# Kernel optimization log

Measured on AMD Instinct MI355X. Metric: run time of the kernel, lower is better.

## Reference

```python
import jax, jax.numpy as jnp
import numpy as np


def setup_inputs() -> dict:
    key = jax.random.key(0)
    ks = jax.random.split(key, 8)
    B, Nq, Nk, D, H, Cv = 8, 4096, 4096, 2, 64, 64
    q = jax.random.normal(ks[0], (B, Nq, D), dtype=jnp.float32)
    k = jax.random.normal(ks[1], (B, Nk, D), dtype=jnp.float32)
    v = jax.random.normal(ks[2], (B, Nk, Cv), dtype=jnp.float32)
    # Linear params (torch nn.Linear layout: W is (out, in), y = x @ W.T + b)
    s = 1.0 / np.sqrt(D)
    q_proj_w = jax.random.uniform(ks[3], (H, D), jnp.float32, -s, s)
    q_proj_b = jax.random.uniform(ks[4], (H,), jnp.float32, -s, s)
    k_proj_w = jax.random.uniform(ks[5], (H, D), jnp.float32, -s, s)
    k_proj_b = jax.random.uniform(ks[6], (H,), jnp.float32, -s, s)
    return {"q": q, "k": k, "v": v,
            "q_proj_w": q_proj_w, "q_proj_b": q_proj_b,
            "k_proj_w": k_proj_w, "k_proj_b": k_proj_b,
            "top_k": 16}


def _cdist(q, k):
    # Euclidean distances (B, Nq, Nk) via the Gram trick (avoids a BxNqxNkxD diff tensor)
    q2 = jnp.sum(q * q, axis=-1)  # (B, Nq)
    k2 = jnp.sum(k * k, axis=-1)  # (B, Nk)
    d2 = q2[:, :, None] + k2[:, None, :] - 2.0 * jnp.einsum('bqd,bnd->bqn', q, k)
    return jnp.sqrt(jnp.maximum(d2, 0.0))


def _batched_gather(inputs, idx):
    # inputs: (B, Nk, C), idx: (B, Nq, K) -> (B, Nq, K, C)
    return jax.vmap(lambda inp, ix: inp[ix])(inputs, idx)


def reference(q, k, v, q_proj_w, q_proj_b, k_proj_w, k_proj_b, top_k):
    dists = _cdist(q, k)                                   # (B, Nq, Nk)
    _, knn_idx = jax.lax.top_k(-dists, top_k)              # smallest distances
    k_knn = _batched_gather(k, knn_idx)                    # (B, Nq, K, D)
    v_knn = _batched_gather(v, knn_idx)                    # (B, Nq, K, Cv)
    q_emb = q @ q_proj_w.T + q_proj_b                      # (B, Nq, H)
    k_emb = k_knn @ k_proj_w.T + k_proj_b                  # (B, Nq, K, H)
    attn_scores = jnp.einsum('bqh,bqkh->bqk', q_emb, k_emb)
    attn = jax.nn.softmax(attn_scores, axis=-1)
    out = jnp.einsum('bqk,bqkc->bqc', attn, v_knn)         # (B, Nq, Cv)
    return out
```

## Files before the change

kernel.cpp:

```cpp
#include <hip/hip_runtime.h>
#include <stdint.h>

typedef uint64_t u64;
typedef uint32_t u32;

#define NB    8
#define NQ    4096
#define NKEY  4096
#define CV    64
#define KSEL  16
#define G     8
#define NWAVE 4
#define BLK   (NWAVE * 64)
#define CMAX  64
#define PADU  (~(u64)0)

__device__ __forceinline__ u64 shflxor_u64(u64 v, int m) {
    const u32 lo = __shfl_xor((int)(u32)v, m);
    const u32 hi = __shfl_xor((int)(u32)(v >> 32), m);
    return (((u64)hi) << 32) | lo;
}
__device__ __forceinline__ int mbcnt64(u64 m) {
    return (int)__builtin_amdgcn_mbcnt_hi((u32)(m >> 32),
               __builtin_amdgcn_mbcnt_lo((u32)m, 0));
}
__device__ __forceinline__ u32 fkey(float f) {
    const u32 b = __float_as_uint(f);
    return b ^ (0x80000000u | (u32)((int32_t)b >> 31));
}

__device__ __forceinline__ float lanesort64_f32(float v, int lane) {
#pragma unroll
    for (int k = 2; k <= 64; k <<= 1) {
#pragma unroll
        for (int j = k >> 1; j > 0; j >>= 1) {
            const float p = __shfl_xor(v, j);
            const bool up    = ((lane & k) == 0);
            const bool lower = ((lane & j) == 0);
            v = (lower == up) ? fminf(v, p) : fmaxf(v, p);
        }
    }
    return v;
}

__device__ __forceinline__ u64 top16of64(u64 v, int lane) {
#pragma unroll
    for (int k = 2; k <= 16; k <<= 1) {
#pragma unroll
        for (int j = k >> 1; j > 0; j >>= 1) {
            const u64 p = shflxor_u64(v, j);
            const bool up    = ((lane & k) == 0);
            const bool lower = ((lane & j) == 0);
            const u64 mn = v < p ? v : p, mx = v < p ? p : v;
            v = (lower == up) ? mn : mx;
        }
    }
    {   const u64 p = shflxor_u64(v, 16);
        const u64 mn = v < p ? v : p, mx = v < p ? p : v;
        v = ((lane & 16) == 0) ? mn : mx; }
#pragma unroll
    for (int j = 8; j > 0; j >>= 1) {
        const u64 p = shflxor_u64(v, j);
        const bool lower = ((lane & j) == 0);
        const bool dasc  = ((lane & 32) == 0);
        const u64 mn = v < p ? v : p, mx = v < p ? p : v;
        v = (lower == dasc) ? mn : mx;
    }
    {   const u64 p = shflxor_u64(v, 32);
        const u64 mn = v < p ? v : p, mx = v < p ? p : v;
        v = ((lane & 32) == 0) ? mn : mx; }
    return v;
}

__global__ void setup_kernel(const float* __restrict__ qw, const float* __restrict__ qb,
                             const float* __restrict__ kw, const float* __restrict__ kb,
                             float* __restrict__ w9)
{
    const int h = threadIdx.x & 63;
    const float2 a = ((const float2*)qw)[h];
    const float2 c = ((const float2*)kw)[h];
    const float qbh = qb[h], kbh = kb[h];
    float s[9] = { a.x * c.x, a.y * c.x, qbh * c.x,
                   a.x * c.y, a.y * c.y, qbh * c.y,
                   a.x * kbh, a.y * kbh, qbh * kbh };
#pragma unroll
    for (int i = 0; i < 9; ++i)
#pragma unroll
        for (int off = 32; off; off >>= 1) s[i] += __shfl_xor(s[i], off);
    if (h == 0) {
#pragma unroll
        for (int i = 0; i < 9; ++i) w9[i] = s[i];
    }
}

extern "C" __global__ __launch_bounds__(BLK, 4) void bev_main(
    const float* __restrict__ qg, const float* __restrict__ kg,
    const float* __restrict__ vg, const float* __restrict__ w9,
    float* __restrict__ outg)
{
    __shared__ u64 cand[NWAVE][G][CMAX];

    const int tid  = threadIdx.x;
    const int wv   = tid >> 6;
    const int lane = tid & 63;
    const int wvu  = __builtin_amdgcn_readfirstlane(wv);
    const int b    = blockIdx.x >> 7;
    const int qbase = ((int)(blockIdx.x & 127) * NWAVE + wvu) * G;

    const float2* kp  = (const float2*)(kg + (size_t)b * NKEY * 2);
    const float4* kp4 = (const float4*)kp;
    const float2* qp  = (const float2*)qg + (size_t)b * NQ + qbase;

    float qxx[G], qyy[G], m2x[G], m2y[G];
#pragma unroll
    for (int q = 0; q < G; ++q) {
        const float2 qc = qp[q];
        qxx[q] = qc.x; qyy[q] = qc.y;
        m2x[q] = -2.f * qc.x; m2y[q] = -2.f * qc.y;
    }

    float mn[G];
#pragma unroll
    for (int q = 0; q < G; ++q) mn[q] = __builtin_inff();
#pragma unroll 8
    for (int c = 0; c < 32; ++c) {
        const float4 kk = kp4[c * 64 + lane];
        const float k2a = fmaf(kk.x, kk.x, kk.y * kk.y);
        const float k2b = fmaf(kk.z, kk.z, kk.w * kk.w);
#pragma unroll
        for (int q = 0; q < G; ++q) {
            const float va = fmaf(kk.x, m2x[q], fmaf(kk.y, m2y[q], k2a));
            const float vb = fmaf(kk.z, m2x[q], fmaf(kk.w, m2y[q], k2b));
            mn[q] = fminf(mn[q], fminf(va, vb));
        }
    }

    float thr[G];
#pragma unroll
    for (int q = 0; q < G; ++q)
        thr[q] = __shfl(lanesort64_f32(mn[q], lane), 15);

    int cnt[G];
#pragma unroll
    for (int q = 0; q < G; ++q) cnt[q] = 0;
#pragma unroll 4
    for (int c = 0; c < 32; ++c) {
        const float4 kk = kp4[c * 64 + lane];
        const float k2a = fmaf(kk.x, kk.x, kk.y * kk.y);
        const float k2b = fmaf(kk.z, kk.z, kk.w * kk.w);
        const u32 ia = (u32)(2 * (c * 64 + lane));
#pragma unroll
        for (int q = 0; q < G; ++q) {
            const float va = fmaf(kk.x, m2x[q], fmaf(kk.y, m2y[q], k2a));
            const float vb = fmaf(kk.z, m2x[q], fmaf(kk.w, m2y[q], k2b));
            const bool aa = va <= thr[q];
            const bool ab = vb <= thr[q];
            const u64 mka = __ballot(aa);
            const u64 mkb = __ballot(ab);
            if (mka | mkb) {
                const int posa = cnt[q] + mbcnt64(mka);
                cnt[q] += (int)__popcll(mka);
                const int posb = cnt[q] + mbcnt64(mkb);
                cnt[q] += (int)__popcll(mkb);
                if (aa && posa < CMAX)
                    cand[wv][q][posa] = (((u64)fkey(va)) << 32) | ia;
                if (ab && posb < CMAX)
                    cand[wv][q][posb] = (((u64)fkey(vb)) << 32) | (ia + 1);
            }
        }
    }

#pragma unroll
    for (int q = 0; q < G; ++q) {
        if (cnt[q] > CMAX) {
            u32 lo = 0, hi = ~0u;
            while (lo < hi) {
                const u32 mid = lo + ((hi - lo) >> 1);
                int cc = 0;
#pragma unroll 1
                for (int c = 0; c < 32; ++c) {
                    const float4 kk = kp4[c * 64 + lane];
                    const float k2a = fmaf(kk.x, kk.x, kk.y * kk.y);
                    const float k2b = fmaf(kk.z, kk.z, kk.w * kk.w);
                    const float va = fmaf(kk.x, m2x[q], fmaf(kk.y, m2y[q], k2a));
                    const float vb = fmaf(kk.z, m2x[q], fmaf(kk.w, m2y[q], k2b));
                    cc += (fkey(va) <= mid) ? 1 : 0;
                    cc += (fkey(vb) <= mid) ? 1 : 0;
                }
#pragma unroll
                for (int off = 32; off; off >>= 1) cc += __shfl_xor(cc, off);
                if (cc >= KSEL) hi = mid; else lo = mid + 1;
            }
            int cc = 0;
#pragma unroll 1
            for (int c = 0; c < 32; ++c) {
                const float4 kk = kp4[c * 64 + lane];
                const float k2a = fmaf(kk.x, kk.x, kk.y * kk.y);
                const float k2b = fmaf(kk.z, kk.z, kk.w * kk.w);
                const float va = fmaf(kk.x, m2x[q], fmaf(kk.y, m2y[q], k2a));
                const float vb = fmaf(kk.z, m2x[q], fmaf(kk.w, m2y[q], k2b));
                const u32 ta = fkey(va), tb = fkey(vb);
                const bool aa = ta <= lo, ab = tb <= lo;
                const u64 mka = __ballot(aa);
                const u64 mkb = __ballot(ab);
                const int posa = cc + mbcnt64(mka);
                cc += (int)__popcll(mka);
                const int posb = cc + mbcnt64(mkb);
                cc += (int)__popcll(mkb);
                const u32 ia = (u32)(2 * (c * 64 + lane));
                if (aa && posa < CMAX) cand[wv][q][posa] = (((u64)ta) << 32) | ia;
                if (ab && posb < CMAX) cand[wv][q][posb] = (((u64)tb) << 32) | (ia + 1);
            }
            cnt[q] = cc < CMAX ? cc : CMAX;
        }
    }

    const float s1 = w9[0], s2 = w9[1], s3 = w9[2];
    const float s4 = w9[3], s5 = w9[4], s6 = w9[5];
    const float s7 = w9[6], s8 = w9[7], s9 = w9[8];
    const float* vb = vg + (size_t)b * NKEY * CV;

#pragma unroll 1
    for (int q = 0; q < G; ++q) {
        u64 myv = (lane < cnt[q]) ? cand[wv][q][lane] : PADU;
        myv = top16of64(myv, lane);
        const u32 myidx = (u32)myv;

        const float A  = fmaf(qxx[q], s1, fmaf(qyy[q], s2, s3));
        const float Bb = fmaf(qxx[q], s4, fmaf(qyy[q], s5, s6));
        const float Cc = fmaf(qxx[q], s7, fmaf(qyy[q], s8, s9));

        const int sel = (lane < KSEL) ? (int)myidx : 0;
        const float2 kc = kp[sel];
        const float score = fmaf(A, kc.x, fmaf(Bb, kc.y, Cc));
        float mx = score;
#pragma unroll
        for (int off = 8; off; off >>= 1) mx = fmaxf(mx, __shfl_xor(mx, off));
        const float e = __expf(score - mx);
        float sum = e;
#pragma unroll
        for (int off = 8; off; off >>= 1) sum += __shfl_xor(sum, off);
        const float w = e / sum;

        float acc = 0.f;
#pragma unroll
        for (int s = 0; s < KSEL; ++s) {
            const u32 id   = (u32)__builtin_amdgcn_readlane((int)myidx, s);
            const float ws = __uint_as_float(
                (u32)__builtin_amdgcn_readlane((int)__float_as_uint(w), s));
            acc = fmaf(ws, vb[(size_t)id * CV + lane], acc);
        }
        outg[((size_t)b * NQ + qbase + q) * CV + lane] = acc;
    }
}

extern "C" void kernel_launch(void* const* d_in, const int* in_sizes, int n_in,
                              void* d_out, int out_size, void* d_ws, size_t ws_size,
                              hipStream_t stream) {
    const float* q  = (const float*)d_in[0];
    const float* k  = (const float*)d_in[1];
    const float* v  = (const float*)d_in[2];
    const float* qw = (const float*)d_in[3];
    const float* qb = (const float*)d_in[4];
    const float* kw = (const float*)d_in[5];
    const float* kb = (const float*)d_in[6];
    float* out = (float*)d_out;
    float* w9  = (float*)d_ws;

    hipLaunchKernelGGL(setup_kernel, dim3(1), dim3(64), 0, stream,
                       qw, qb, kw, kb, w9);
    hipLaunchKernelGGL(bev_main, dim3(NB * NQ / (G * NWAVE)), dim3(BLK),
                       0, stream, q, k, v, w9, out);
}
```

Measured before the change: 74.86 us.

## Replace brute-force kNN scan with Morton-sorted key chunks and bbox pruning

Adds a setup kernel that bins keys into a 64x64 grid, sorts them by Morton order into 64 chunks of 64, and records per-chunk bounding boxes. The main kernel gives each wave one query, seeds a top-16 from the nearest chunk, then scans only chunks whose bbox lower bound is within the current 16th distance. This removes the full scan over all 4096 keys per query. In exchange it adds a sort pass, a fixed grid range assumption of [-4,4) (exactness is kept by clamping), and data-dependent irregular work.

```diff
diff --git a/kernel.cpp b/kernel.cpp
--- a/kernel.cpp
+++ b/kernel.cpp
@@ -3,17 +3,22 @@
 
 typedef uint64_t u64;
 typedef uint32_t u32;
+typedef unsigned short u16;
 
 #define NB    8
 #define NQ    4096
 #define NKEY  4096
 #define CV    64
 #define KSEL  16
-#define G     8
-#define NWAVE 4
-#define BLK   (NWAVE * 64)
-#define CMAX  64
+#define GRD   64
+#define NCELL (GRD * GRD)
+#define NCHUNK 64
+#define CMAX  128
 #define PADU  (~(u64)0)
+
+#define WS_SKEY  256
+#define WS_SIDX  (WS_SKEY + NB * NKEY * 8)
+#define WS_BBOX  (WS_SIDX + NB * NKEY * 2)
 
 __device__ __forceinline__ u64 shflxor_u64(u64 v, int m) {
     const u32 lo = __shfl_xor((int)(u32)v, m);
@@ -24,23 +29,16 @@
     return (int)__builtin_amdgcn_mbcnt_hi((u32)(m >> 32),
                __builtin_amdgcn_mbcnt_lo((u32)m, 0));
 }
-__device__ __forceinline__ u32 fkey(float f) {
-    const u32 b = __float_as_uint(f);
-    return b ^ (0x80000000u | (u32)((int32_t)b >> 31));
-}
-
-__device__ __forceinline__ float lanesort64_f32(float v, int lane) {
-#pragma unroll
-    for (int k = 2; k <= 64; k <<= 1) {
-#pragma unroll
-        for (int j = k >> 1; j > 0; j >>= 1) {
-            const float p = __shfl_xor(v, j);
-            const bool up    = ((lane & k) == 0);
-            const bool lower = ((lane & j) == 0);
-            v = (lower == up) ? fminf(v, p) : fmaxf(v, p);
-        }
-    }
-    return v;
+__device__ __forceinline__ int cellof(float x) {
+    int c = (int)floorf((x + 4.0f) * 8.0f);
+    return c < 0 ? 0 : (c > GRD - 1 ? GRD - 1 : c);
+}
+__device__ __forceinline__ u32 part1by1(u32 x) {
+    x &= 0xFFu;
+    x = (x | (x << 4)) & 0x0F0Fu;
+    x = (x | (x << 2)) & 0x3333u;
+    x = (x | (x << 1)) & 0x5555u;
+    return x;
 }
 
 __device__ __forceinline__ u64 top16of64(u64 v, int lane) {
@@ -72,186 +70,233 @@
     return v;
 }
 
-__global__ void setup_kernel(const float* __restrict__ qw, const float* __restrict__ qb,
-                             const float* __restrict__ kw, const float* __restrict__ kb,
-                             float* __restrict__ w9)
+__global__ __launch_bounds__(1024, 1) void k_setup(
+    const float* __restrict__ kg,
+    const float* __restrict__ qw, const float* __restrict__ qb,
+    const float* __restrict__ kw, const float* __restrict__ kb,
+    float2* __restrict__ skey_g, u16* __restrict__ sidx_g,
+    float4* __restrict__ bbox_g, float* __restrict__ w9)
 {
-    const int h = threadIdx.x & 63;
-    const float2 a = ((const float2*)qw)[h];
-    const float2 c = ((const float2*)kw)[h];
-    const float qbh = qb[h], kbh = kb[h];
-    float s[9] = { a.x * c.x, a.y * c.x, qbh * c.x,
-                   a.x * c.y, a.y * c.y, qbh * c.y,
-                   a.x * kbh, a.y * kbh, qbh * kbh };
-#pragma unroll
-    for (int i = 0; i < 9; ++i)
-#pragma unroll
-        for (int off = 32; off; off >>= 1) s[i] += __shfl_xor(s[i], off);
-    if (h == 0) {
-#pragma unroll
-        for (int i = 0; i < 9; ++i) w9[i] = s[i];
-    }
-}
-
-extern "C" __global__ __launch_bounds__(BLK, 4) void bev_main(
+    __shared__ u32    hist[NCELL];
+    __shared__ float2 skl[NKEY];
+    __shared__ u16    sil[NKEY];
+    __shared__ u32    wtot[16];
+
+    const int b = blockIdx.x, t = threadIdx.x;
+    const int wv = t >> 6, lane = t & 63;
+
+#pragma unroll
+    for (int i = 0; i < 4; ++i) hist[t * 4 + i] = 0u;
+    __syncthreads();
+
+    float2 kk[4]; int cel[4];
+#pragma unroll
+    for (int i = 0; i < 4; ++i) {
+        const int gid = t + i * 1024;
+        kk[i] = ((const float2*)kg)[(size_t)b * NKEY + gid];
+        cel[i] = (int)(part1by1((u32)cellof(kk[i].x)) |
+                       (part1by1((u32)cellof(kk[i].y)) << 1));
+        atomicAdd(&hist[cel[i]], 1u);
+    }
+    __syncthreads();
+
+    const u32 h0 = hist[4 * t], h1 = hist[4 * t + 1];
+    const u32 h2 = hist[4 * t + 2], h3 = hist[4 * t + 3];
+    const u32 s = h0 + h1 + h2 + h3;
+    u32 inc = s;
+#pragma unroll
+    for (int off = 1; off < 64; off <<= 1) {
+        const u32 p = __shfl_up(inc, off);
+        if (lane >= off) inc += p;
+    }
+    if (lane == 63) wtot[wv] = inc;
+    __syncthreads();
+    if (wv == 0 && lane < 16) {
+        const u32 v = wtot[lane];
+        u32 sc = v;
+#pragma unroll
+        for (int off = 1; off < 16; off <<= 1) {
+            const u32 p = __shfl_up(sc, off);
+            if (lane >= off) sc += p;
+        }
+        wtot[lane] = sc - v;
+    }
+    __syncthreads();
+    const u32 base = wtot[wv] + (inc - s);
+    hist[4 * t]     = base;
+    hist[4 * t + 1] = base + h0;
+    hist[4 * t + 2] = base + h0 + h1;
+    hist[4 * t + 3] = base + h0 + h1 + h2;
+    __syncthreads();
+
+#pragma unroll
+    for (int i = 0; i < 4; ++i) {
+        const u32 p = atomicAdd(&hist[cel[i]], 1u);
+        skl[p] = kk[i];
+        sil[p] = (u16)(t + i * 1024);
+    }
+    __syncthreads();
+
+    float2* skb = skey_g + (size_t)b * NKEY;
+    u16*    sib = sidx_g + (size_t)b * NKEY;
+#pragma unroll
+    for (int i = 0; i < 4; ++i) {
+        const int g = t + i * 1024;
+        skb[g] = skl[g];
+        sib[g] = sil[g];
+    }
+#pragma unroll
+    for (int j = 0; j < 4; ++j) {
+        const int ch = wv * 4 + j;
+        const float2 kc = skl[ch * 64 + lane];
+        float xlo = kc.x, xhi = kc.x, ylo = kc.y, yhi = kc.y;
+#pragma unroll
+        for (int off = 32; off; off >>= 1) {
+            xlo = fminf(xlo, __shfl_xor(xlo, off));
+            xhi = fmaxf(xhi, __shfl_xor(xhi, off));
+            ylo = fminf(ylo, __shfl_xor(ylo, off));
+            yhi = fmaxf(yhi, __shfl_xor(yhi, off));
+        }
+        if (lane == 0) bbox_g[b * NCHUNK + ch] = make_float4(xlo, ylo, xhi, yhi);
+    }
+
+    if (b == 0 && t < 64) {
+        const int h = t;
+        const float2 a = ((const float2*)qw)[h];
+        const float2 c = ((const float2*)kw)[h];
+        const float qbh = qb[h], kbh = kb[h];
+        float ss[9] = { a.x * c.x, a.y * c.x, qbh * c.x,
+                        a.x * c.y, a.y * c.y, qbh * c.y,
+                        a.x * kbh, a.y * kbh, qbh * kbh };
+#pragma unroll
+        for (int i = 0; i < 9; ++i)
+#pragma unroll
+            for (int off = 32; off; off >>= 1) ss[i] += __shfl_xor(ss[i], off);
+        if (h == 0) {
+#pragma unroll
+            for (int i = 0; i < 9; ++i) w9[i] = ss[i];
+        }
+    }
+}
+
+extern "C" __global__ __launch_bounds__(256, 8) void bev_knn(
     const float* __restrict__ qg, const float* __restrict__ kg,
     const float* __restrict__ vg, const float* __restrict__ w9,
-    float* __restrict__ outg)
+    const float2* __restrict__ skey_g, const u16* __restrict__ sidx_g,
+    const float4* __restrict__ bbox_g, float* __restrict__ outg)
 {
-    __shared__ u64 cand[NWAVE][G][CMAX];
-
-    const int tid  = threadIdx.x;
-    const int wv   = tid >> 6;
-    const int lane = tid & 63;
-    const int wvu  = __builtin_amdgcn_readfirstlane(wv);
-    const int b    = blockIdx.x >> 7;
-    const int qbase = ((int)(blockIdx.x & 127) * NWAVE + wvu) * G;
-
-    const float2* kp  = (const float2*)(kg + (size_t)b * NKEY * 2);
-    const float4* kp4 = (const float4*)kp;
-    const float2* qp  = (const float2*)qg + (size_t)b * NQ + qbase;
-
-    float qxx[G], qyy[G], m2x[G], m2y[G];
-#pragma unroll
-    for (int q = 0; q < G; ++q) {
-        const float2 qc = qp[q];
-        qxx[q] = qc.x; qyy[q] = qc.y;
-        m2x[q] = -2.f * qc.x; m2y[q] = -2.f * qc.y;
-    }
-
-    float mn[G];
-#pragma unroll
-    for (int q = 0; q < G; ++q) mn[q] = __builtin_inff();
-#pragma unroll 8
-    for (int c = 0; c < 32; ++c) {
-        const float4 kk = kp4[c * 64 + lane];
-        const float k2a = fmaf(kk.x, kk.x, kk.y * kk.y);
-        const float k2b = fmaf(kk.z, kk.z, kk.w * kk.w);
-#pragma unroll
-        for (int q = 0; q < G; ++q) {
-            const float va = fmaf(kk.x, m2x[q], fmaf(kk.y, m2y[q], k2a));
-            const float vb = fmaf(kk.z, m2x[q], fmaf(kk.w, m2y[q], k2b));
-            mn[q] = fminf(mn[q], fminf(va, vb));
-        }
-    }
-
-    float thr[G];
-#pragma unroll
-    for (int q = 0; q < G; ++q)
-        thr[q] = __shfl(lanesort64_f32(mn[q], lane), 15);
-
-    int cnt[G];
-#pragma unroll
-    for (int q = 0; q < G; ++q) cnt[q] = 0;
-#pragma unroll 4
-    for (int c = 0; c < 32; ++c) {
-        const float4 kk = kp4[c * 64 + lane];
-        const float k2a = fmaf(kk.x, kk.x, kk.y * kk.y);
-        const float k2b = fmaf(kk.z, kk.z, kk.w * kk.w);
-        const u32 ia = (u32)(2 * (c * 64 + lane));
-#pragma unroll
-        for (int q = 0; q < G; ++q) {
-            const float va = fmaf(kk.x, m2x[q], fmaf(kk.y, m2y[q], k2a));
-            const float vb = fmaf(kk.z, m2x[q], fmaf(kk.w, m2y[q], k2b));
-            const bool aa = va <= thr[q];
-            const bool ab = vb <= thr[q];
-            const u64 mka = __ballot(aa);
-            const u64 mkb = __ballot(ab);
-            if (mka | mkb) {
-                const int posa = cnt[q] + mbcnt64(mka);
-                cnt[q] += (int)__popcll(mka);
-                const int posb = cnt[q] + mbcnt64(mkb);
-                cnt[q] += (int)__popcll(mkb);
-                if (aa && posa < CMAX)
-                    cand[wv][q][posa] = (((u64)fkey(va)) << 32) | ia;
-                if (ab && posb < CMAX)
-                    cand[wv][q][posb] = (((u64)fkey(vb)) << 32) | (ia + 1);
+    __shared__ u64 cand[4][CMAX];
+
+    const int tid = threadIdx.x, wv = tid >> 6, lane = tid & 63;
+    const int gw = blockIdx.x * 4 + wv;
+    const int b  = gw >> 12, qi = gw & 4095;
+
+    const float2 qc = ((const float2*)qg)[(size_t)b * NQ + qi];
+    const float qx = qc.x, qy = qc.y;
+    const float2* sk = skey_g + (size_t)b * NKEY;
+    const u16*    si = sidx_g + (size_t)b * NKEY;
+    u64* cd = cand[wv];
+
+    const float4 bb = bbox_g[b * NCHUNK + lane];
+    const float dx = fmaxf(fmaxf(bb.x - qx, qx - bb.z), 0.f);
+    const float dy = fmaxf(fmaxf(bb.y - qy, qy - bb.w), 0.f);
+    const float bd = fmaf(dx, dx, dy * dy);
+
+    float bmn = bd;
+#pragma unroll
+    for (int off = 32; off; off >>= 1) bmn = fminf(bmn, __shfl_xor(bmn, off));
+    const int cn = __builtin_ctzll((unsigned long long)__ballot(bd == bmn));
+
+    u64 myv;
+    {
+        const int pos = cn * 64 + lane;
+        const float2 kk = sk[pos];
+        const float ddx = qx - kk.x, ddy = qy - kk.y;
+        const float d2 = fmaf(ddx, ddx, ddy * ddy);
+        myv = (((u64)__float_as_uint(d2)) << 32) | (u32)si[pos];
+    }
+    myv = top16of64(myv, lane);
+
+    u64 b16;
+    {
+        u64 m = (lane < KSEL) ? myv : 0;
+#pragma unroll
+        for (int off = 32; off; off >>= 1) { const u64 p = shflxor_u64(m, off); m = p > m ? p : m; }
+        b16 = m;
+    }
+    float d16f = __uint_as_float((u32)(b16 >> 32));
+
+    u64 mask = __ballot(bd <= d16f) & ~(1ull << cn);
+    int ecnt = 0;
+#pragma unroll 1
+    while (mask) {
+        const int c = __builtin_ctzll((unsigned long long)mask);
+        mask &= mask - 1;
+        const int pos = c * 64 + lane;
+        const float2 kk = sk[pos];
+        const float ddx = qx - kk.x, ddy = qy - kk.y;
+        const float d2 = fmaf(ddx, ddx, ddy * ddy);
+        const u64 pk = (((u64)__float_as_uint(d2)) << 32) | (u32)si[pos];
+        const bool acc = pk < b16;
+        const u64 mk = __ballot(acc);
+        if (mk) {
+            const int p = ecnt + mbcnt64(mk);
+            if (acc) cd[p] = pk;
+            ecnt += (int)__popcll(mk);
+            if (ecnt >= CMAX - 64) {
+#pragma unroll 1
+                while (ecnt > 0) {
+                    const int take = ecnt < 48 ? ecnt : 48;
+                    const u64 inv = (lane < KSEL) ? myv
+                                  : ((lane - KSEL < take) ? cd[ecnt - take + lane - KSEL] : PADU);
+                    myv = top16of64(inv, lane);
+                    ecnt -= take;
+                }
+                u64 m = (lane < KSEL) ? myv : 0;
+#pragma unroll
+                for (int off = 32; off; off >>= 1) { const u64 p2 = shflxor_u64(m, off); m = p2 > m ? p2 : m; }
+                b16 = m; d16f = __uint_as_float((u32)(b16 >> 32));
+                mask &= __ballot(bd <= d16f);
             }
         }
     }
-
-#pragma unroll
-    for (int q = 0; q < G; ++q) {
-        if (cnt[q] > CMAX) {
-            u32 lo = 0, hi = ~0u;
-            while (lo < hi) {
-                const u32 mid = lo + ((hi - lo) >> 1);
-                int cc = 0;
 #pragma unroll 1
-                for (int c = 0; c < 32; ++c) {
-                    const float4 kk = kp4[c * 64 + lane];
-                    const float k2a = fmaf(kk.x, kk.x, kk.y * kk.y);
-                    const float k2b = fmaf(kk.z, kk.z, kk.w * kk.w);
-                    const float va = fmaf(kk.x, m2x[q], fmaf(kk.y, m2y[q], k2a));
-                    const float vb = fmaf(kk.z, m2x[q], fmaf(kk.w, m2y[q], k2b));
-                    cc += (fkey(va) <= mid) ? 1 : 0;
-                    cc += (fkey(vb) <= mid) ? 1 : 0;
-                }
-#pragma unroll
-                for (int off = 32; off; off >>= 1) cc += __shfl_xor(cc, off);
-                if (cc >= KSEL) hi = mid; else lo = mid + 1;
-            }
-            int cc = 0;
-#pragma unroll 1
-            for (int c = 0; c < 32; ++c) {
-                const float4 kk = kp4[c * 64 + lane];
-                const float k2a = fmaf(kk.x, kk.x, kk.y * kk.y);
-                const float k2b = fmaf(kk.z, kk.z, kk.w * kk.w);
-                const float va = fmaf(kk.x, m2x[q], fmaf(kk.y, m2y[q], k2a));
-                const float vb = fmaf(kk.z, m2x[q], fmaf(kk.w, m2y[q], k2b));
-                const u32 ta = fkey(va), tb = fkey(vb);
-                const bool aa = ta <= lo, ab = tb <= lo;
-                const u64 mka = __ballot(aa);
-                const u64 mkb = __ballot(ab);
-                const int posa = cc + mbcnt64(mka);
-                cc += (int)__popcll(mka);
-                const int posb = cc + mbcnt64(mkb);
-                cc += (int)__popcll(mkb);
-                const u32 ia = (u32)(2 * (c * 64 + lane));
-                if (aa && posa < CMAX) cand[wv][q][posa] = (((u64)ta) << 32) | ia;
-                if (ab && posb < CMAX) cand[wv][q][posb] = (((u64)tb) << 32) | (ia + 1);
-            }
-            cnt[q] = cc < CMAX ? cc : CMAX;
-        }
-    }
-
-    const float s1 = w9[0], s2 = w9[1], s3 = w9[2];
-    const float s4 = w9[3], s5 = w9[4], s6 = w9[5];
-    const float s7 = w9[6], s8 = w9[7], s9 = w9[8];
+    while (ecnt > 0) {
+        const int take = ecnt < 48 ? ecnt : 48;
+        const u64 inv = (lane < KSEL) ? myv
+                      : ((lane - KSEL < take) ? cd[ecnt - take + lane - KSEL] : PADU);
+        myv = top16of64(inv, lane);
+        ecnt -= take;
+    }
+
+    const u32 myidx = (u32)myv;
+    const float A  = fmaf(qx, w9[0], fmaf(qy, w9[1], w9[2]));
+    const float Bb = fmaf(qx, w9[3], fmaf(qy, w9[4], w9[5]));
+    const float Cc = fmaf(qx, w9[6], fmaf(qy, w9[7], w9[8]));
+
+    const float2* kp = (const float2*)kg + (size_t)b * NKEY;
+    const int sel = (lane < KSEL) ? (int)myidx : 0;
+    const float2 kc = kp[sel];
+    const float score = fmaf(A, kc.x, fmaf(Bb, kc.y, Cc));
+    float mx = score;
+#pragma unroll
+    for (int off = 8; off; off >>= 1) mx = fmaxf(mx, __shfl_xor(mx, off));
+    const float e = __expf(score - mx);
+    float sum = e;
+#pragma unroll
+    for (int off = 8; off; off >>= 1) sum += __shfl_xor(sum, off);
+    const float w = e / sum;
+
     const float* vb = vg + (size_t)b * NKEY * CV;
-
-#pragma unroll 1
-    for (int q = 0; q < G; ++q) {
-        u64 myv = (lane < cnt[q]) ? cand[wv][q][lane] : PADU;
-        myv = top16of64(myv, lane);
-        const u32 myidx = (u32)myv;
-
-        const float A  = fmaf(qxx[q], s1, fmaf(qyy[q], s2, s3));
-        const float Bb = fmaf(qxx[q], s4, fmaf(qyy[q], s5, s6));
-        const float Cc = fmaf(qxx[q], s7, fmaf(qyy[q], s8, s9));
-
-        const int sel = (lane < KSEL) ? (int)myidx : 0;
-        const float2 kc = kp[sel];
-        const float score = fmaf(A, kc.x, fmaf(Bb, kc.y, Cc));
-        float mx = score;
-#pragma unroll
-        for (int off = 8; off; off >>= 1) mx = fmaxf(mx, __shfl_xor(mx, off));
-        const float e = __expf(score - mx);
-        float sum = e;
-#pragma unroll
-        for (int off = 8; off; off >>= 1) sum += __shfl_xor(sum, off);
-        const float w = e / sum;
-
-        float acc = 0.f;
-#pragma unroll
-        for (int s = 0; s < KSEL; ++s) {
-            const u32 id   = (u32)__builtin_amdgcn_readlane((int)myidx, s);
-            const float ws = __uint_as_float(
-                (u32)__builtin_amdgcn_readlane((int)__float_as_uint(w), s));
-            acc = fmaf(ws, vb[(size_t)id * CV + lane], acc);
-        }
-        outg[((size_t)b * NQ + qbase + q) * CV + lane] = acc;
-    }
+    float acc = 0.f;
+#pragma unroll
+    for (int sct = 0; sct < KSEL; ++sct) {
+        const u32 id   = (u32)__builtin_amdgcn_readlane((int)myidx, sct);
+        const float ws = __uint_as_float(
+            (u32)__builtin_amdgcn_readlane((int)__float_as_uint(w), sct));
+        acc = fmaf(ws, vb[(size_t)id * CV + lane], acc);
+    }
+    outg[((size_t)b * NQ + qi) * CV + lane] = acc;
 }
 
 extern "C" void kernel_launch(void* const* d_in, const int* in_sizes, int n_in,
@@ -265,10 +310,14 @@
     const float* kw = (const float*)d_in[5];
     const float* kb = (const float*)d_in[6];
     float* out = (float*)d_out;
-    float* w9  = (float*)d_ws;
-
-    hipLaunchKernelGGL(setup_kernel, dim3(1), dim3(64), 0, stream,
-                       qw, qb, kw, kb, w9);
-    hipLaunchKernelGGL(bev_main, dim3(NB * NQ / (G * NWAVE)), dim3(BLK),
-                       0, stream, q, k, v, w9, out);
-}
+
+    float*  w9   = (float*)d_ws;
+    float2* skey = (float2*)((char*)d_ws + WS_SKEY);
+    u16*    sidx = (u16*)((char*)d_ws + WS_SIDX);
+    float4* bbox = (float4*)((char*)d_ws + WS_BBOX);
+
+    hipLaunchKernelGGL(k_setup, dim3(NB), dim3(1024), 0, stream,
+                       k, qw, qb, kw, kb, skey, sidx, bbox, w9);
+    hipLaunchKernelGGL(bev_knn, dim3(NB * NQ / 4), dim3(256), 0, stream,
+                       q, k, v, w9, skey, sidx, bbox, out);
+}
```

New measurement: 161.8 us. 116% more time.
